# Performance work log

Hardware: AMD Instinct MI355X
Metric: run time of the kernel (lower is better)

Reference implementation:

```python
import jax, jax.numpy as jnp
import numpy as np
import math

B, S, D, H = 4, 1024, 1024, 16
DK = D // H


def setup_inputs() -> dict:
    key = jax.random.key(0)
    ks = jax.random.split(key, 14)
    inp = {
        "query": jax.random.normal(ks[0], (B, S, D), dtype=jnp.float32),
        "key": jax.random.normal(ks[1], (B, S, D), dtype=jnp.float32),
        "value": jax.random.normal(ks[2], (B, S, D), dtype=jnp.float32),
        "attention_bias": jax.random.normal(ks[3], (B, S, S, H), dtype=jnp.float32),
        "mask": jax.random.randint(ks[4], (B, S), 0, 2).astype(bool),
    }
    scale = 0.02
    inp["Wq"] = jax.random.normal(ks[5], (D, D), dtype=jnp.float32) * scale
    inp["bq"] = jnp.zeros((D,), dtype=jnp.float32)
    inp["Wk"] = jax.random.normal(ks[6], (D, D), dtype=jnp.float32) * scale
    inp["bk"] = jnp.zeros((D,), dtype=jnp.float32)
    inp["Wv"] = jax.random.normal(ks[7], (D, D), dtype=jnp.float32) * scale
    inp["bv"] = jnp.zeros((D,), dtype=jnp.float32)
    inp["Wo"] = jax.random.normal(ks[8], (D, D), dtype=jnp.float32) * scale
    inp["bo"] = jnp.zeros((D,), dtype=jnp.float32)
    return inp


def reference(query, key, value, attention_bias, mask, Wq, bq, Wk, bk, Wv, bv, Wo, bo):
    # projections (torch Linear: x @ W.T + b), split heads -> [B,H,S,DK]
    def proj(x, W, b):
        y = x @ W.T + b
        return y.reshape(B, S, H, DK).transpose(0, 2, 1, 3)

    q = proj(query, Wq, bq)
    k = proj(key, Wk, bk)
    v = proj(value, Wv, bv)

    bias = attention_bias.transpose(0, 3, 1, 2)  # [B,H,S,S]
    scores = (jnp.einsum("bhqd,bhkd->bhqk", q, k) + bias) / math.sqrt(DK)

    # pairwise mask: outer product of per-token mask, broadcast over heads
    pm = (mask[:, None, :, None] & mask[:, None, None, :])  # [B,1,S,S]
    scores = jnp.where(pm, scores, jnp.float32(-1e9))

    p_attn = jax.nn.softmax(scores, axis=-1)  # dropout is identity in eval
    x = jnp.einsum("bhqk,bhkd->bhqd", p_attn, v)
    x = x.transpose(0, 2, 1, 3).reshape(B, S, D)
    return x @ Wo.T + bo
```

## Files before the change

kernel.cpp:

```cpp
#include <hip/hip_runtime.h>
#include <hip/hip_bf16.h>
#include <math.h>

#define B_ 4
#define S_ 1024
#define D_ 1024
#define H_ 16
#define DK_ 64

typedef short bf16x8 __attribute__((ext_vector_type(8)));
typedef float f32x4 __attribute__((ext_vector_type(4)));

#define MFMA(a, b, c) __builtin_amdgcn_mfma_f32_16x16x32_bf16(a, b, c, 0, 0, 0)

#define GLDS(gp, lp)                                                        \
    __builtin_amdgcn_global_load_lds(                                       \
        (const __attribute__((address_space(1))) void*)(const void*)(gp),   \
        (__attribute__((address_space(3))) void*)(void*)(lp), 16, 0, 0)

static __device__ __forceinline__ unsigned short f2bf(float f) {
    __hip_bfloat16 h = __float2bfloat16(f);
    return *reinterpret_cast<unsigned short*>(&h);
}
static __device__ __forceinline__ float bf2f(unsigned short u) {
    unsigned int x = ((unsigned int)u) << 16;
    union { unsigned int i; float f; } c; c.i = x; return c.f;
}

__global__ __launch_bounds__(256) void cvt_all(
    const float* __restrict__ a, const float* __restrict__ b, const float* __restrict__ c,
    const float* __restrict__ wa, const float* __restrict__ wb,
    const float* __restrict__ wc, const float* __restrict__ wd,
    unsigned short* __restrict__ oa, unsigned short* __restrict__ ob, unsigned short* __restrict__ oc,
    unsigned short* __restrict__ owa, unsigned short* __restrict__ owb,
    unsigned short* __restrict__ owc, unsigned short* __restrict__ owd)
{
    int bx = blockIdx.x;
    const float* in; unsigned short* out; int i;
    if (bx < 12288) {
        int which = bx >> 12;
        in  = which == 0 ? a : which == 1 ? b : c;
        out = which == 0 ? oa : which == 1 ? ob : oc;
        i = (bx & 4095) * 256 + threadIdx.x;
    } else {
        int b2 = bx - 12288;
        int which = b2 >> 10;
        in  = which == 0 ? wa : which == 1 ? wb : which == 2 ? wc : wd;
        out = which == 0 ? owa : which == 1 ? owb : which == 2 ? owc : owd;
        i = (b2 & 1023) * 256 + threadIdx.x;
    }
    float4 v = ((const float4*)in)[i];
    ushort4 o;
    o.x = f2bf(v.x); o.y = f2bf(v.y); o.z = f2bf(v.z); o.w = f2bf(v.w);
    ((ushort4*)out)[i] = o;
}

__global__ __launch_bounds__(256, 2) void qkv_prep(
    const unsigned short* __restrict__ X0, const unsigned short* __restrict__ X1,
    const unsigned short* __restrict__ X2,
    const unsigned short* __restrict__ W0, const unsigned short* __restrict__ W1,
    const unsigned short* __restrict__ W2,
    const float* __restrict__ bv0, const float* __restrict__ bv1,
    const float* __restrict__ bv2,
    unsigned short* __restrict__ Y0, unsigned short* __restrict__ Y1,
    unsigned short* __restrict__ Y2,
    const float* __restrict__ bias, const int* __restrict__ mask,
    unsigned short* __restrict__ biasP)
{
    __shared__ unsigned short As[128 * 32];
    __shared__ unsigned short Bs[128 * 32];

    const int t = threadIdx.x;
    const int bid = blockIdx.x;
    const int grp = bid / 19, rr = bid - grp * 19;

    if (rr < 3) {
        const int gi = grp * 3 + rr;
        const int z = gi >> 8;
        const int rem = gi & 255;
        const int n0 = (rem & 7) * 128, m0 = (rem >> 3) * 128;

        const unsigned short* X = z == 0 ? X0 : z == 1 ? X1 : X2;
        const unsigned short* W = z == 0 ? W0 : z == 1 ? W1 : W2;
        const float* bvec = z == 0 ? bv0 : z == 1 ? bv1 : bv2;
        unsigned short* Y = z == 0 ? Y0 : z == 1 ? Y1 : Y2;

        const int w = t >> 6, l = t & 63;
        const int lane16 = l & 15, quad = l >> 4;
        const int wr = w >> 1, wc = w & 1;

        const int srow = w * 16 + (l >> 2);
        const unsigned short* agp = X + (size_t)(m0 + srow) * 1024 + (l & 3) * 8;
        const unsigned short* bgp = W + (size_t)(n0 + srow) * 1024 + (l & 3) * 8;
        unsigned short* alp = As + w * 512 + l * 8;
        unsigned short* blp = Bs + w * 512 + l * 8;

        f32x4 zero = {0.f, 0.f, 0.f, 0.f};
        f32x4 acc[4][4];
        #pragma unroll
        for (int i = 0; i < 4; ++i)
            #pragma unroll
            for (int j = 0; j < 4; ++j) acc[i][j] = zero;

        for (int kt = 0; kt < 1024; kt += 32) {
            GLDS(agp + kt, alp);
            GLDS(agp + kt + 64 * 1024, alp + 2048);
            GLDS(bgp + kt, blp);
            GLDS(bgp + kt + 64 * 1024, blp + 2048);
            __syncthreads();

            bf16x8 af[4], bfv[4];
            #pragma unroll
            for (int i = 0; i < 4; ++i)
                af[i] = *(const bf16x8*)(As + (wr * 64 + i * 16 + lane16) * 32 + quad * 8);
            #pragma unroll
            for (int j = 0; j < 4; ++j)
                bfv[j] = *(const bf16x8*)(Bs + (wc * 64 + j * 16 + lane16) * 32 + quad * 8);

            #pragma unroll
            for (int i = 0; i < 4; ++i)
                #pragma unroll
                for (int j = 0; j < 4; ++j)
                    acc[i][j] = MFMA(af[i], bfv[j], acc[i][j]);
            __syncthreads();
        }

        float bvl[4];
        #pragma unroll
        for (int j = 0; j < 4; ++j) bvl[j] = bvec[n0 + wc * 64 + j * 16 + lane16];

        if (z == 2) {
            const int bb = m0 >> 10;
            const int sb = (m0 & 1023) + wr * 64;
            #pragma unroll
            for (int i = 0; i < 4; ++i) {
                #pragma unroll
                for (int j = 0; j < 4; ++j) {
                    int n = n0 + wc * 64 + j * 16 + lane16;
                    ushort4 pk;
                    pk.x = f2bf(acc[i][j][0] + bvl[j]);
                    pk.y = f2bf(acc[i][j][1] + bvl[j]);
                    pk.z = f2bf(acc[i][j][2] + bvl[j]);
                    pk.w = f2bf(acc[i][j][3] + bvl[j]);
                    int s = sb + i * 16 + quad * 4;
                    *(ushort4*)(Y + ((size_t)(bb * 1024 + n)) * 1024 + s) = pk;
                }
            }
        } else {
            #pragma unroll
            for (int i = 0; i < 4; ++i) {
                int mrow[4];
                #pragma unroll
                for (int r = 0; r < 4; ++r)
                    mrow[r] = (z == 0) ? mask[m0 + wr * 64 + i * 16 + quad * 4 + r] : 1;
                #pragma unroll
                for (int j = 0; j < 4; ++j) {
                    int n = n0 + wc * 64 + j * 16 + lane16;
                    #pragma unroll
                    for (int r = 0; r < 4; ++r) {
                        size_t m = m0 + wr * 64 + i * 16 + quad * 4 + r;
                        float val = acc[i][j][r] + bvl[j];
                        if (z == 0) val = mrow[r] ? val * 0.125f : 0.f;
                        Y[m * 1024 + n] = f2bf(val);
                    }
                }
            }
        }
    } else {
        const int pidx = grp * 16 + (rr - 3);
        const int hh = t & 15, u = t >> 4;
        const int kt = pidx & 15, q16 = (pidx >> 4) & 63, bb = pidx >> 10;

        const unsigned short NEG = f2bf(-28672.f);

        int mk[4];
        #pragma unroll
        for (int j = 0; j < 4; ++j) mk[j] = mask[bb * 1024 + kt * 64 + j * 16 + u];

        const float* bbp = bias + (((size_t)(bb * 1024 + q16 * 16) * 1024) + kt * 64) * 16 + hh;
        unsigned short* obp = biasP + ((((size_t)(bb * 16 + hh) * 64 + q16) * 16 + kt) * 64) * 16;

        #pragma unroll
        for (int quad = 0; quad < 4; ++quad) {
            bf16x8 v0, v1;
            #pragma unroll
            for (int r = 0; r < 4; ++r) {
                int q = quad * 4 + r;
                int mq = mask[bb * 1024 + q16 * 16 + q];
                #pragma unroll
                for (int j = 0; j < 4; ++j) {
                    float v = bbp[((size_t)q * 1024 + j * 16 + u) * 16];
                    unsigned short pv = (mq && mk[j]) ? f2bf(v * 0.125f) : NEG;
                    if (j < 2) v0[j * 4 + r] = (short)pv;
                    else       v1[(j - 2) * 4 + r] = (short)pv;
                }
            }
            unsigned short* dst = obp + (size_t)(quad * 16 + u) * 16;
            *(bf16x8*)(dst) = v0;
            *(bf16x8*)(dst + 8) = v1;
        }
    }
}

__global__ __launch_bounds__(256, 2) void attn_mfma(
    const unsigned short* __restrict__ Qp, const unsigned short* __restrict__ Kp,
    const unsigned short* __restrict__ VpT, const unsigned short* __restrict__ biasP,
    unsigned short* __restrict__ Xp)
{
    __shared__ unsigned short Ks[2][64 * 64];
    __shared__ unsigned short Vs[2][64 * 64];
    __shared__ unsigned short Ps[4][16 * 64];

    const int t = threadIdx.x;
    const int w = t >> 6, l = t & 63;
    const int lane16 = l & 15, quad = l >> 4;

    const int bid = blockIdx.x;
    const int bh = bid & 63, qt = bid >> 6;
    const int h = bh & 15, b = bh >> 4;
    const int q0 = qt * 64;
    const int qrow0 = q0 + w * 16;
    const int q16 = qt * 4 + w;

    bf16x8 qf[2];
    #pragma unroll
    for (int c = 0; c < 2; ++c)
        qf[c] = *(const bf16x8*)(Qp + (size_t)(b * 1024 + qrow0 + lane16) * 1024
                                 + h * 64 + c * 32 + quad * 8);

    const unsigned short* bp = biasP
        + ((((size_t)(b * 16 + h) * 64 + q16) * 16) * 64 + l) * 16;

    const int krow = w * 8 + (l >> 3);
    const int kgran = (l & 7) ^ ((l >> 3) & 7);
    const unsigned short* kg = Kp + (size_t)(b * 1024 + krow) * 1024 + h * 64 + kgran * 8;
    const unsigned short* vg = VpT + ((size_t)(b * 16 + h) * 64 + krow) * 1024 + kgran * 8;
    unsigned short* kst = &Ks[0][w * 512 + l * 8];
    unsigned short* vst = &Vs[0][w * 512 + l * 8];

    GLDS(kg, kst);
    GLDS(kg + (size_t)32 * 1024, kst + 32 * 64);
    GLDS(vg, vst);
    GLDS(vg + (size_t)32 * 1024, vst + 32 * 64);
    bf16x8 bfr0 = *(const bf16x8*)(bp);
    bf16x8 bfr1 = *(const bf16x8*)(bp + 8);

    f32x4 zero = {0.f, 0.f, 0.f, 0.f};
    f32x4 o[4];
    #pragma unroll
    for (int j = 0; j < 4; ++j) o[j] = zero;
    float m_i[4] = {-1e30f, -1e30f, -1e30f, -1e30f};
    float l_i[4] = {0.f, 0.f, 0.f, 0.f};

    char* psb = (char*)&Ps[w][0];

    for (int kt16 = 0; kt16 < 16; ++kt16) {
        const int cur = kt16 & 1;
        __syncthreads();

        if (kt16 < 15) {
            const size_t kn = (size_t)(kt16 + 1) * 64;
            unsigned short* kd = kst + (cur ^ 1) * 4096;
            unsigned short* vd = vst + (cur ^ 1) * 4096;
            GLDS(kg + kn * 1024, kd);
            GLDS(kg + (kn + 32) * 1024, kd + 32 * 64);
            GLDS(vg + kn, vd);
            GLDS(vg + kn + (size_t)32 * 1024, vd + 32 * 64);
        }

        const unsigned short* Kc = &Ks[0][0] + cur * 4096;
        const unsigned short* Vc = &Vs[0][0] + cur * 4096;

        f32x4 s[4];
        #pragma unroll
        for (int j = 0; j < 4; ++j) {
            s[j] = zero;
            #pragma unroll
            for (int c = 0; c < 2; ++c) {
                bf16x8 kf = *(const bf16x8*)(Kc + (j * 16 + lane16) * 64
                                             + (((c * 4 + quad) ^ (lane16 & 7)) * 8));
                s[j] = MFMA(qf[c], kf, s[j]);
            }
        }

        #pragma unroll
        for (int e = 0; e < 8; ++e) {
            s[e >> 2][e & 3]       += bf2f((unsigned short)bfr0[e]);
            s[2 + (e >> 2)][e & 3] += bf2f((unsigned short)bfr1[e]);
        }

        if (kt16 < 15) {
            bfr0 = *(const bf16x8*)(bp + (size_t)(kt16 + 1) * 1024);
            bfr1 = *(const bf16x8*)(bp + (size_t)(kt16 + 1) * 1024 + 8);
        }

        float p[4][4];
        #pragma unroll
        for (int r = 0; r < 4; ++r) {
            float mx = fmaxf(fmaxf(s[0][r], s[1][r]), fmaxf(s[2][r], s[3][r]));
            #pragma unroll
            for (int d = 1; d < 16; d <<= 1) mx = fmaxf(mx, __shfl_xor(mx, d, 64));
            float mnew = fmaxf(m_i[r], mx);
            float alpha = __expf(m_i[r] - mnew);
            m_i[r] = mnew;
            float sum = 0.f;
            #pragma unroll
            for (int j = 0; j < 4; ++j) {
                p[j][r] = __expf(s[j][r] - mnew);
                sum += p[j][r];
            }
            #pragma unroll
            for (int d = 1; d < 16; d <<= 1) sum += __shfl_xor(sum, d, 64);
            l_i[r] = l_i[r] * alpha + sum;
            #pragma unroll
            for (int jd = 0; jd < 4; ++jd) o[jd][r] *= alpha;
        }

        #pragma unroll
        for (int j = 0; j < 4; ++j)
            #pragma unroll
            for (int r = 0; r < 4; ++r) {
                int row = quad * 4 + r;
                int cb = (j * 16 + lane16) * 2;
                *(unsigned short*)(psb + row * 128 + (cb ^ ((row & 7) << 4))) = f2bf(p[j][r]);
            }
        asm volatile("" ::: "memory");

        bf16x8 pf[2];
        #pragma unroll
        for (int c = 0; c < 2; ++c) {
            int cb = c * 64 + quad * 16;
            pf[c] = *(const bf16x8*)(psb + lane16 * 128 + (cb ^ ((lane16 & 7) << 4)));
        }

        #pragma unroll
        for (int jd = 0; jd < 4; ++jd)
            #pragma unroll
            for (int c = 0; c < 2; ++c) {
                bf16x8 vf = *(const bf16x8*)(Vc + (jd * 16 + lane16) * 64
                                             + (((c * 4 + quad) ^ (lane16 & 7)) * 8));
                o[jd] = MFMA(pf[c], vf, o[jd]);
            }
    }

    float inv[4];
    #pragma unroll
    for (int r = 0; r < 4; ++r) inv[r] = 1.0f / l_i[r];

    #pragma unroll
    for (int jd = 0; jd < 4; ++jd)
        #pragma unroll
        for (int r = 0; r < 4; ++r)
            Xp[(size_t)(b * 1024 + qrow0 + quad * 4 + r) * 1024
               + h * 64 + jd * 16 + lane16] = f2bf(o[jd][r] * inv[r]);
}

__global__ __launch_bounds__(256, 2) void gemm_o64(
    const unsigned short* __restrict__ X, const unsigned short* __restrict__ W,
    const float* __restrict__ bvec, float* __restrict__ Y)
{
    __shared__ unsigned short As[128 * 32];
    __shared__ unsigned short Bs[64 * 32];

    const int t = threadIdx.x;
    const int w = t >> 6, l = t & 63;
    const int lane16 = l & 15, quad = l >> 4;
    const int m0 = blockIdx.y * 128, n0 = blockIdx.x * 64;
    const int wr = w >> 1, wc = w & 1;

    const int srow = w * 16 + (l >> 2);
    const unsigned short* agp = X + (size_t)(m0 + srow) * 1024 + (l & 3) * 8;
    const unsigned short* bgp = W + (size_t)(n0 + srow) * 1024 + (l & 3) * 8;
    unsigned short* alp = As + w * 512 + l * 8;
    unsigned short* blp = Bs + w * 512 + l * 8;

    f32x4 zero = {0.f, 0.f, 0.f, 0.f};
    f32x4 acc[4][2];
    #pragma unroll
    for (int i = 0; i < 4; ++i)
        #pragma unroll
        for (int j = 0; j < 2; ++j) acc[i][j] = zero;

    for (int kt = 0; kt < 1024; kt += 32) {
        GLDS(agp + kt, alp);
        GLDS(agp + kt + 64 * 1024, alp + 2048);
        GLDS(bgp + kt, blp);
        __syncthreads();

        bf16x8 af[4], bfv[2];
        #pragma unroll
        for (int i = 0; i < 4; ++i)
            af[i] = *(const bf16x8*)(As + (wr * 64 + i * 16 + lane16) * 32 + quad * 8);
        #pragma unroll
        for (int j = 0; j < 2; ++j)
            bfv[j] = *(const bf16x8*)(Bs + (wc * 32 + j * 16 + lane16) * 32 + quad * 8);

        #pragma unroll
        for (int i = 0; i < 4; ++i)
            #pragma unroll
            for (int j = 0; j < 2; ++j)
                acc[i][j] = MFMA(af[i], bfv[j], acc[i][j]);
        __syncthreads();
    }

    float bvl[2];
    #pragma unroll
    for (int j = 0; j < 2; ++j) bvl[j] = bvec[n0 + wc * 32 + j * 16 + lane16];

    #pragma unroll
    for (int i = 0; i < 4; ++i)
        #pragma unroll
        for (int j = 0; j < 2; ++j) {
            int n = n0 + wc * 32 + j * 16 + lane16;
            #pragma unroll
            for (int r = 0; r < 4; ++r) {
                size_t m = m0 + wr * 64 + i * 16 + quad * 4 + r;
                Y[m * 1024 + n] = acc[i][j][r] + bvl[j];
            }
        }
}

extern "C" void kernel_launch(void* const* d_in, const int* in_sizes, int n_in,
                              void* d_out, int out_size, void* d_ws, size_t ws_size,
                              hipStream_t stream)
{
    const float* query = (const float*)d_in[0];
    const float* key   = (const float*)d_in[1];
    const float* value = (const float*)d_in[2];
    const float* abias = (const float*)d_in[3];
    const int*   mask  = (const int*)d_in[4];
    const float* Wq = (const float*)d_in[5];
    const float* bq = (const float*)d_in[6];
    const float* Wk = (const float*)d_in[7];
    const float* bk = (const float*)d_in[8];
    const float* Wv = (const float*)d_in[9];
    const float* bv = (const float*)d_in[10];
    const float* Wo = (const float*)d_in[11];
    const float* bo = (const float*)d_in[12];
    float* out = (float*)d_out;

    const size_t T = (size_t)B_ * S_ * D_;
    const size_t WSZ = (size_t)D_ * D_;
    const size_t BPSZ = (size_t)B_ * H_ * S_ * S_;
    unsigned short* p = (unsigned short*)d_ws;
    unsigned short* biasP = p;  p += BPSZ;
    unsigned short* qb  = p;  p += T;
    unsigned short* kb  = p;  p += T;
    unsigned short* vb  = p;  p += T;
    unsigned short* wqb = p;  p += WSZ;
    unsigned short* wkb = p;  p += WSZ;
    unsigned short* wvb = p;  p += WSZ;
    unsigned short* wob = p;  p += WSZ;
    unsigned short* Qpj = p;  p += T;
    unsigned short* Kpj = p;  p += T;
    unsigned short* VpT = p;  p += T;
    unsigned short* Xpj = p;  p += T;

    cvt_all<<<dim3(16384), 256, 0, stream>>>(
        query, key, value, Wq, Wk, Wv, Wo,
        qb, kb, vb, wqb, wkb, wvb, wob);

    qkv_prep<<<dim3(4864), 256, 0, stream>>>(
        qb, kb, vb, wqb, wkb, wvb, bq, bk, bv,
        Qpj, Kpj, VpT, abias, mask, biasP);

    attn_mfma<<<dim3(1024), 256, 0, stream>>>(Qpj, Kpj, VpT, biasP, Xpj);

    gemm_o64<<<dim3(16, 32), 256, 0, stream>>>(Xpj, wob, bo, out);
}
```

Before: 601.7 us.

## Split bias prep from QKV GEMM, fold bias into MFMA init, MFMA row sums

The fused qkv_prep kernel, which interleaved GEMM blocks with bias-permute blocks, is split into two separate launches: prep_bias and a 3D-grid gemm128. In attention, the bias tile now seeds the QK^T MFMA accumulator instead of being added afterwards. The softmax row sum is computed by an MFMA against a ones vector rather than cross-lane shuffles. s_setprio raises wave priority around the MFMA blocks. These changes trade one extra launch and lost overlap between the bandwidth-bound bias pass and the compute-bound GEMM for fewer shuffle and VALU instructions in the attention inner loop.

Result: faster. 561.4 us (-6.7%).

```diff
diff --git a/kernel.cpp b/kernel.cpp
--- a/kernel.cpp
+++ b/kernel.cpp
@@ -55,7 +55,46 @@
     ((ushort4*)out)[i] = o;
 }
 
-__global__ __launch_bounds__(256, 2) void qkv_prep(
+__global__ __launch_bounds__(256) void prep_bias(
+    const float* __restrict__ bias, const int* __restrict__ mask,
+    unsigned short* __restrict__ biasP)
+{
+    const int t = threadIdx.x;
+    const int h = t & 15, u = t >> 4;
+    const int x = blockIdx.x;
+    const int kt = x & 15, q16 = (x >> 4) & 63, b = x >> 10;
+
+    const unsigned short NEG = f2bf(-28672.f);
+
+    int mk[4];
+    #pragma unroll
+    for (int j = 0; j < 4; ++j) mk[j] = mask[b * 1024 + kt * 64 + j * 16 + u];
+
+    const float* bb = bias + (((size_t)(b * 1024 + q16 * 16) * 1024) + kt * 64) * 16 + h;
+    unsigned short* ob = biasP + ((((size_t)(b * 16 + h) * 64 + q16) * 16 + kt) * 64) * 16;
+
+    #pragma unroll
+    for (int quad = 0; quad < 4; ++quad) {
+        bf16x8 v0, v1;
+        #pragma unroll
+        for (int r = 0; r < 4; ++r) {
+            int q = quad * 4 + r;
+            int mq = mask[b * 1024 + q16 * 16 + q];
+            #pragma unroll
+            for (int j = 0; j < 4; ++j) {
+                float v = bb[((size_t)q * 1024 + j * 16 + u) * 16];
+                unsigned short pv = (mq && mk[j]) ? f2bf(v * 0.125f) : NEG;
+                if (j < 2) v0[j * 4 + r] = (short)pv;
+                else       v1[(j - 2) * 4 + r] = (short)pv;
+            }
+        }
+        unsigned short* dst = ob + (size_t)(quad * 16 + u) * 16;
+        *(bf16x8*)(dst) = v0;
+        *(bf16x8*)(dst + 8) = v1;
+    }
+}
+
+__global__ __launch_bounds__(256, 2) void gemm128(
     const unsigned short* __restrict__ X0, const unsigned short* __restrict__ X1,
     const unsigned short* __restrict__ X2,
     const unsigned short* __restrict__ W0, const unsigned short* __restrict__ W1,
@@ -64,140 +103,98 @@
     const float* __restrict__ bv2,
     unsigned short* __restrict__ Y0, unsigned short* __restrict__ Y1,
     unsigned short* __restrict__ Y2,
-    const float* __restrict__ bias, const int* __restrict__ mask,
-    unsigned short* __restrict__ biasP)
+    const int* __restrict__ mask)
 {
     __shared__ unsigned short As[128 * 32];
     __shared__ unsigned short Bs[128 * 32];
 
+    const int z = blockIdx.z;
+    const unsigned short* X = z == 0 ? X0 : z == 1 ? X1 : X2;
+    const unsigned short* W = z == 0 ? W0 : z == 1 ? W1 : W2;
+    const float* bvec = z == 0 ? bv0 : z == 1 ? bv1 : bv2;
+    unsigned short* Y = z == 0 ? Y0 : z == 1 ? Y1 : Y2;
+
     const int t = threadIdx.x;
-    const int bid = blockIdx.x;
-    const int grp = bid / 19, rr = bid - grp * 19;
-
-    if (rr < 3) {
-        const int gi = grp * 3 + rr;
-        const int z = gi >> 8;
-        const int rem = gi & 255;
-        const int n0 = (rem & 7) * 128, m0 = (rem >> 3) * 128;
-
-        const unsigned short* X = z == 0 ? X0 : z == 1 ? X1 : X2;
-        const unsigned short* W = z == 0 ? W0 : z == 1 ? W1 : W2;
-        const float* bvec = z == 0 ? bv0 : z == 1 ? bv1 : bv2;
-        unsigned short* Y = z == 0 ? Y0 : z == 1 ? Y1 : Y2;
-
-        const int w = t >> 6, l = t & 63;
-        const int lane16 = l & 15, quad = l >> 4;
-        const int wr = w >> 1, wc = w & 1;
-
-        const int srow = w * 16 + (l >> 2);
-        const unsigned short* agp = X + (size_t)(m0 + srow) * 1024 + (l & 3) * 8;
-        const unsigned short* bgp = W + (size_t)(n0 + srow) * 1024 + (l & 3) * 8;
-        unsigned short* alp = As + w * 512 + l * 8;
-        unsigned short* blp = Bs + w * 512 + l * 8;
-
-        f32x4 zero = {0.f, 0.f, 0.f, 0.f};
-        f32x4 acc[4][4];
+    const int w = t >> 6, l = t & 63;
+    const int lane16 = l & 15, quad = l >> 4;
+    const int m0 = blockIdx.y * 128, n0 = blockIdx.x * 128;
+    const int wr = w >> 1, wc = w & 1;
+
+    const int srow = w * 16 + (l >> 2);
+    const unsigned short* agp = X + (size_t)(m0 + srow) * 1024 + (l & 3) * 8;
+    const unsigned short* bgp = W + (size_t)(n0 + srow) * 1024 + (l & 3) * 8;
+    unsigned short* alp = As + w * 512 + l * 8;
+    unsigned short* blp = Bs + w * 512 + l * 8;
+
+    f32x4 zero = {0.f, 0.f, 0.f, 0.f};
+    f32x4 acc[4][4];
+    #pragma unroll
+    for (int i = 0; i < 4; ++i)
+        #pragma unroll
+        for (int j = 0; j < 4; ++j) acc[i][j] = zero;
+
+    for (int kt = 0; kt < 1024; kt += 32) {
+        GLDS(agp + kt, alp);
+        GLDS(agp + kt + 64 * 1024, alp + 2048);
+        GLDS(bgp + kt, blp);
+        GLDS(bgp + kt + 64 * 1024, blp + 2048);
+        __syncthreads();
+
+        bf16x8 af[4], bfv[4];
         #pragma unroll
         for (int i = 0; i < 4; ++i)
-            #pragma unroll
-            for (int j = 0; j < 4; ++j) acc[i][j] = zero;
-
-        for (int kt = 0; kt < 1024; kt += 32) {
-            GLDS(agp + kt, alp);
-            GLDS(agp + kt + 64 * 1024, alp + 2048);
-            GLDS(bgp + kt, blp);
-            GLDS(bgp + kt + 64 * 1024, blp + 2048);
-            __syncthreads();
-
-            bf16x8 af[4], bfv[4];
-            #pragma unroll
-            for (int i = 0; i < 4; ++i)
-                af[i] = *(const bf16x8*)(As + (wr * 64 + i * 16 + lane16) * 32 + quad * 8);
+            af[i] = *(const bf16x8*)(As + (wr * 64 + i * 16 + lane16) * 32 + quad * 8);
+        #pragma unroll
+        for (int j = 0; j < 4; ++j)
+            bfv[j] = *(const bf16x8*)(Bs + (wc * 64 + j * 16 + lane16) * 32 + quad * 8);
+
+        #pragma unroll
+        for (int i = 0; i < 4; ++i)
             #pragma unroll
             for (int j = 0; j < 4; ++j)
-                bfv[j] = *(const bf16x8*)(Bs + (wc * 64 + j * 16 + lane16) * 32 + quad * 8);
-
-            #pragma unroll
-            for (int i = 0; i < 4; ++i)
+                acc[i][j] = MFMA(af[i], bfv[j], acc[i][j]);
+        __syncthreads();
+    }
+
+    float bvl[4];
+    #pragma unroll
+    for (int j = 0; j < 4; ++j) bvl[j] = bvec[n0 + wc * 64 + j * 16 + lane16];
+
+    if (z == 2) {
+        const int bb = m0 >> 10;
+        const int sb = (m0 & 1023) + wr * 64;
+        #pragma unroll
+        for (int i = 0; i < 4; ++i) {
+            #pragma unroll
+            for (int j = 0; j < 4; ++j) {
+                int n = n0 + wc * 64 + j * 16 + lane16;
+                ushort4 pk;
+                pk.x = f2bf(acc[i][j][0] + bvl[j]);
+                pk.y = f2bf(acc[i][j][1] + bvl[j]);
+                pk.z = f2bf(acc[i][j][2] + bvl[j]);
+                pk.w = f2bf(acc[i][j][3] + bvl[j]);
+                int s = sb + i * 16 + quad * 4;
+                *(ushort4*)(Y + ((size_t)(bb * 1024 + n)) * 1024 + s) = pk;
+            }
+        }
+    } else {
+        #pragma unroll
+        for (int i = 0; i < 4; ++i) {
+            int mrow[4];
+            #pragma unroll
+            for (int r = 0; r < 4; ++r)
+                mrow[r] = (z == 0) ? mask[m0 + wr * 64 + i * 16 + quad * 4 + r] : 1;
+            #pragma unroll
+            for (int j = 0; j < 4; ++j) {
+                int n = n0 + wc * 64 + j * 16 + lane16;
                 #pragma unroll
-                for (int j = 0; j < 4; ++j)
-                    acc[i][j] = MFMA(af[i], bfv[j], acc[i][j]);
-            __syncthreads();
-        }
-
-        float bvl[4];
-        #pragma unroll
-        for (int j = 0; j < 4; ++j) bvl[j] = bvec[n0 + wc * 64 + j * 16 + lane16];
-
-        if (z == 2) {
-            const int bb = m0 >> 10;
-            const int sb = (m0 & 1023) + wr * 64;
-            #pragma unroll
-            for (int i = 0; i < 4; ++i) {
-                #pragma unroll
-                for (int j = 0; j < 4; ++j) {
-                    int n = n0 + wc * 64 + j * 16 + lane16;
-                    ushort4 pk;
-                    pk.x = f2bf(acc[i][j][0] + bvl[j]);
-                    pk.y = f2bf(acc[i][j][1] + bvl[j]);
-                    pk.z = f2bf(acc[i][j][2] + bvl[j]);
-                    pk.w = f2bf(acc[i][j][3] + bvl[j]);
-                    int s = sb + i * 16 + quad * 4;
-                    *(ushort4*)(Y + ((size_t)(bb * 1024 + n)) * 1024 + s) = pk;
+                for (int r = 0; r < 4; ++r) {
+                    size_t m = m0 + wr * 64 + i * 16 + quad * 4 + r;
+                    float val = acc[i][j][r] + bvl[j];
+                    if (z == 0) val = mrow[r] ? val * 0.125f : 0.f;
+                    Y[m * 1024 + n] = f2bf(val);
                 }
             }
-        } else {
-            #pragma unroll
-            for (int i = 0; i < 4; ++i) {
-                int mrow[4];
-                #pragma unroll
-                for (int r = 0; r < 4; ++r)
-                    mrow[r] = (z == 0) ? mask[m0 + wr * 64 + i * 16 + quad * 4 + r] : 1;
-                #pragma unroll
-                for (int j = 0; j < 4; ++j) {
-                    int n = n0 + wc * 64 + j * 16 + lane16;
-                    #pragma unroll
-                    for (int r = 0; r < 4; ++r) {
-                        size_t m = m0 + wr * 64 + i * 16 + quad * 4 + r;
-                        float val = acc[i][j][r] + bvl[j];
-                        if (z == 0) val = mrow[r] ? val * 0.125f : 0.f;
-                        Y[m * 1024 + n] = f2bf(val);
-                    }
-                }
-            }
-        }
-    } else {
-        const int pidx = grp * 16 + (rr - 3);
-        const int hh = t & 15, u = t >> 4;
-        const int kt = pidx & 15, q16 = (pidx >> 4) & 63, bb = pidx >> 10;
-
-        const unsigned short NEG = f2bf(-28672.f);
-
-        int mk[4];
-        #pragma unroll
-        for (int j = 0; j < 4; ++j) mk[j] = mask[bb * 1024 + kt * 64 + j * 16 + u];
-
-        const float* bbp = bias + (((size_t)(bb * 1024 + q16 * 16) * 1024) + kt * 64) * 16 + hh;
-        unsigned short* obp = biasP + ((((size_t)(bb * 16 + hh) * 64 + q16) * 16 + kt) * 64) * 16;
-
-        #pragma unroll
-        for (int quad = 0; quad < 4; ++quad) {
-            bf16x8 v0, v1;
-            #pragma unroll
-            for (int r = 0; r < 4; ++r) {
-                int q = quad * 4 + r;
-                int mq = mask[bb * 1024 + q16 * 16 + q];
-                #pragma unroll
-                for (int j = 0; j < 4; ++j) {
-                    float v = bbp[((size_t)q * 1024 + j * 16 + u) * 16];
-                    unsigned short pv = (mq && mk[j]) ? f2bf(v * 0.125f) : NEG;
-                    if (j < 2) v0[j * 4 + r] = (short)pv;
-                    else       v1[(j - 2) * 4 + r] = (short)pv;
-                }
-            }
-            unsigned short* dst = obp + (size_t)(quad * 16 + u) * 16;
-            *(bf16x8*)(dst) = v0;
-            *(bf16x8*)(dst + 8) = v1;
         }
     }
 }
@@ -218,8 +215,7 @@
     const int bid = blockIdx.x;
     const int bh = bid & 63, qt = bid >> 6;
     const int h = bh & 15, b = bh >> 4;
-    const int q0 = qt * 64;
-    const int qrow0 = q0 + w * 16;
+    const int qrow0 = qt * 64 + w * 16;
     const int q16 = qt * 4 + w;
 
     bf16x8 qf[2];
@@ -227,6 +223,10 @@
     for (int c = 0; c < 2; ++c)
         qf[c] = *(const bf16x8*)(Qp + (size_t)(b * 1024 + qrow0 + lane16) * 1024
                                  + h * 64 + c * 32 + quad * 8);
+
+    bf16x8 ones;
+    #pragma unroll
+    for (int e = 0; e < 8; ++e) ones[e] = (short)0x3F80;
 
     const unsigned short* bp = biasP
         + ((((size_t)(b * 16 + h) * 64 + q16) * 16) * 64 + l) * 16;
@@ -273,8 +273,16 @@
 
         f32x4 s[4];
         #pragma unroll
+        for (int j = 0; j < 2; ++j)
+            #pragma unroll
+            for (int r = 0; r < 4; ++r) {
+                s[j][r]     = bf2f((unsigned short)bfr0[j * 4 + r]);
+                s[2 + j][r] = bf2f((unsigned short)bfr1[j * 4 + r]);
+            }
+
+        __builtin_amdgcn_s_setprio(1);
+        #pragma unroll
         for (int j = 0; j < 4; ++j) {
-            s[j] = zero;
             #pragma unroll
             for (int c = 0; c < 2; ++c) {
                 bf16x8 kf = *(const bf16x8*)(Kc + (j * 16 + lane16) * 64
@@ -282,12 +290,7 @@
                 s[j] = MFMA(qf[c], kf, s[j]);
             }
         }
-
-        #pragma unroll
-        for (int e = 0; e < 8; ++e) {
-            s[e >> 2][e & 3]       += bf2f((unsigned short)bfr0[e]);
-            s[2 + (e >> 2)][e & 3] += bf2f((unsigned short)bfr1[e]);
-        }
+        __builtin_amdgcn_s_setprio(0);
 
         if (kt16 < 15) {
             bfr0 = *(const bf16x8*)(bp + (size_t)(kt16 + 1) * 1024);
@@ -295,6 +298,7 @@
         }
 
         float p[4][4];
+        float alpha_r[4];
         #pragma unroll
         for (int r = 0; r < 4; ++r) {
             float mx = fmaxf(fmaxf(s[0][r], s[1][r]), fmaxf(s[2][r], s[3][r]));
@@ -303,15 +307,9 @@
             float mnew = fmaxf(m_i[r], mx);
             float alpha = __expf(m_i[r] - mnew);
             m_i[r] = mnew;
-            float sum = 0.f;
-            #pragma unroll
-            for (int j = 0; j < 4; ++j) {
-                p[j][r] = __expf(s[j][r] - mnew);
-                sum += p[j][r];
-            }
-            #pragma unroll
-            for (int d = 1; d < 16; d <<= 1) sum += __shfl_xor(sum, d, 64);
-            l_i[r] = l_i[r] * alpha + sum;
+            alpha_r[r] = alpha;
+            #pragma unroll
+            for (int j = 0; j < 4; ++j) p[j][r] = __expf(s[j][r] - mnew);
             #pragma unroll
             for (int jd = 0; jd < 4; ++jd) o[jd][r] *= alpha;
         }
@@ -333,6 +331,8 @@
             pf[c] = *(const bf16x8*)(psb + lane16 * 128 + (cb ^ ((lane16 & 7) << 4)));
         }
 
+        f32x4 lacc = zero;
+        __builtin_amdgcn_s_setprio(1);
         #pragma unroll
         for (int jd = 0; jd < 4; ++jd)
             #pragma unroll
@@ -341,6 +341,14 @@
                                              + (((c * 4 + quad) ^ (lane16 & 7)) * 8));
                 o[jd] = MFMA(pf[c], vf, o[jd]);
             }
+        #pragma unroll
+        for (int c = 0; c < 2; ++c)
+            lacc = MFMA(pf[c], ones, lacc);
+        __builtin_amdgcn_s_setprio(0);
+
+        #pragma unroll
+        for (int r = 0; r < 4; ++r)
+            l_i[r] = l_i[r] * alpha_r[r] + lacc[r];
     }
 
     float inv[4];
@@ -460,9 +468,11 @@
         query, key, value, Wq, Wk, Wv, Wo,
         qb, kb, vb, wqb, wkb, wvb, wob);
 
-    qkv_prep<<<dim3(4864), 256, 0, stream>>>(
+    prep_bias<<<dim3(4096), 256, 0, stream>>>(abias, mask, biasP);
+
+    gemm128<<<dim3(8, 32, 3), 256, 0, stream>>>(
         qb, kb, vb, wqb, wkb, wvb, bq, bk, bv,
-        Qpj, Kpj, VpT, abias, mask, biasP);
+        Qpj, Kpj, VpT, mask);
 
     attn_mfma<<<dim3(1024), 256, 0, stream>>>(Qpj, Kpj, VpT, biasP, Xpj);
 
```
